# Performance work log

Measured on AMD Instinct MI355X. Metric: run time of the kernel, lower is better.

## Reference

```python
import jax, jax.numpy as jnp
import numpy as np

NUM_CODE = 256
DIM_CODE = 64
IMG_DIM = 3 * 32 * 32  # 3072
HID = 16384


def vq(x, codebook, noise_level, key):
    # x: [B, 64], codebook: [256, 64]
    # torch.cdist p=2 -> euclidean distances [B, 256]
    x2 = jnp.sum(x * x, axis=1, keepdims=True)            # [B,1]
    c2 = jnp.sum(codebook * codebook, axis=1)             # [256]
    d = jnp.sqrt(jnp.maximum(x2 - 2.0 * (x @ codebook.T) + c2, 0.0))
    r = jax.nn.softmax(-d / jnp.sqrt(jnp.float32(DIM_CODE)), axis=1)
    noise = jax.random.uniform(key, r.shape, dtype=r.dtype)
    idx = jnp.argmax(r - noise_level * noise, axis=1)
    one_hot = jax.nn.one_hot(idx, NUM_CODE, dtype=r.dtype)
    # straight-through: forward = one_hot, grad flows through r
    r_ste = r - jax.lax.stop_gradient(r - one_hot)
    return r_ste @ codebook                               # [B, 64]


def setup_inputs() -> dict:
    key = jax.random.key(0)
    ks = jax.random.split(key, 10)
    B = 4096
    inp = {
        "x": jax.random.normal(ks[0], (B, 3, 32, 32), dtype=jnp.float32),
        "wb1_encoder": jax.random.normal(ks[1], (IMG_DIM + 1, HID), dtype=jnp.float32) / np.sqrt(IMG_DIM).astype(np.float32),
        "wb2_encoder": jax.random.normal(ks[2], (HID + 1, 4 * DIM_CODE), dtype=jnp.float32) / 128.0,
        "wb1_decoder": jax.random.normal(ks[3], (4 * DIM_CODE + 1, HID), dtype=jnp.float32) / np.sqrt(4 * DIM_CODE).astype(np.float32),
        "wb2_decoder": jax.random.normal(ks[4], (HID + 1, IMG_DIM), dtype=jnp.float32) / 128.0,
        "codebook1": jax.random.normal(ks[5], (NUM_CODE, DIM_CODE), dtype=jnp.float32),
        "codebook2": jax.random.normal(ks[6], (NUM_CODE, DIM_CODE), dtype=jnp.float32),
        "codebook3": jax.random.normal(ks[7], (NUM_CODE, DIM_CODE), dtype=jnp.float32),
        "codebook4": jax.random.normal(ks[8], (NUM_CODE, DIM_CODE), dtype=jnp.float32),
        "noise_level": 1,
    }
    return inp


def reference(x, wb1_encoder, wb2_encoder, wb1_decoder, wb2_decoder,
              codebook1, codebook2, codebook3, codebook4, noise_level):
    nkey = jax.random.key(12345)
    h = jnp.tanh(x.reshape(-1, IMG_DIM) @ wb1_encoder[:-1] + wb1_encoder[-1])
    h = jnp.tanh(h @ wb2_encoder[:-1] + wb2_encoder[-1])      # [B, 256]
    x1, x2, x3, x4 = jnp.split(h, 4, axis=1)                  # each [B, 64]
    # NOTE: source uses codebook1 for all four chunks (faithful to original)
    y1 = vq(x1, codebook1, noise_level, jax.random.fold_in(nkey, 1))
    y2 = vq(x2, codebook1, noise_level, jax.random.fold_in(nkey, 2))
    y3 = vq(x3, codebook1, noise_level, jax.random.fold_in(nkey, 3))
    y4 = vq(x4, codebook1, noise_level, jax.random.fold_in(nkey, 4))
    y = jnp.concatenate((y1, y2, y3, y4), axis=1)             # [B, 256]
    y = jnp.tanh(y @ wb1_decoder[:-1] + wb1_decoder[-1])
    y = y @ wb2_decoder[:-1] + wb2_decoder[-1]
    return y.reshape(-1, 3, 32, 32)
```

## Files before the change

### kernel.cpp

```cpp
#include <hip/hip_runtime.h>
#include <stdint.h>


#define IMG_DIM 3072
#define HID     16384
#define NCODE   256
#define DCODE   64

typedef short bf16x8 __attribute__((ext_vector_type(8)));
typedef float f32x4 __attribute__((ext_vector_type(4)));

__device__ __forceinline__ uint16_t bf16rne(float f) {
    uint32_t u = __float_as_uint(f);
    return (uint16_t)((u + 0x7fffu + ((u >> 16) & 1u)) >> 16);
}
__device__ __forceinline__ float b2f(uint16_t h) {
    return __uint_as_float((uint32_t)h << 16);
}

#define GLLDS(g, l)                                                        \
    __builtin_amdgcn_global_load_lds(                                      \
        (const __attribute__((address_space(1))) uint32_t*)(const void*)(g), \
        (__attribute__((address_space(3))) uint32_t*)(void*)(l), 16, 0, 0)

__host__ __device__ __forceinline__ uint32_t rotl32(uint32_t v, int d) {
    return (v << d) | (v >> (32 - d));
}

__host__ __device__ __forceinline__ void tf2x32(uint32_t k0, uint32_t k1,
                                                uint32_t& x0, uint32_t& x1) {
    uint32_t k2 = k0 ^ k1 ^ 0x1BD11BDAu;
    x0 += k0; x1 += k1;
    x0 += x1; x1 = rotl32(x1, 13); x1 ^= x0;
    x0 += x1; x1 = rotl32(x1, 15); x1 ^= x0;
    x0 += x1; x1 = rotl32(x1, 26); x1 ^= x0;
    x0 += x1; x1 = rotl32(x1,  6); x1 ^= x0;
    x0 += k1; x1 += k2 + 1u;
    x0 += x1; x1 = rotl32(x1, 17); x1 ^= x0;
    x0 += x1; x1 = rotl32(x1, 29); x1 ^= x0;
    x0 += x1; x1 = rotl32(x1, 16); x1 ^= x0;
    x0 += x1; x1 = rotl32(x1, 24); x1 ^= x0;
    x0 += k2; x1 += k0 + 2u;
    x0 += x1; x1 = rotl32(x1, 13); x1 ^= x0;
    x0 += x1; x1 = rotl32(x1, 15); x1 ^= x0;
    x0 += x1; x1 = rotl32(x1, 26); x1 ^= x0;
    x0 += x1; x1 = rotl32(x1,  6); x1 ^= x0;
    x0 += k0; x1 += k1 + 3u;
    x0 += x1; x1 = rotl32(x1, 17); x1 ^= x0;
    x0 += x1; x1 = rotl32(x1, 29); x1 ^= x0;
    x0 += x1; x1 = rotl32(x1, 16); x1 ^= x0;
    x0 += x1; x1 = rotl32(x1, 24); x1 ^= x0;
    x0 += k1; x1 += k2 + 4u;
    x0 += x1; x1 = rotl32(x1, 13); x1 ^= x0;
    x0 += x1; x1 = rotl32(x1, 15); x1 ^= x0;
    x0 += x1; x1 = rotl32(x1, 26); x1 ^= x0;
    x0 += x1; x1 = rotl32(x1,  6); x1 ^= x0;
    x0 += k2; x1 += k0 + 5u;
}

template <int EPI, bool SPLIT>
__global__ __launch_bounds__(256) void gemm_mfma(
    const uint16_t* __restrict__ Ahi, const uint16_t* __restrict__ Alo,
    const uint16_t* __restrict__ Bhi, const uint16_t* __restrict__ Blo,
    const float* __restrict__ biasp,
    float* __restrict__ Cf, uint16_t* __restrict__ Cb,
    uint16_t* __restrict__ Chi, uint16_t* __restrict__ Clo,
    int M, int N, int K) {
    constexpr int AT = 128 * 32;
    __shared__ __align__(16) uint16_t As[SPLIT ? 2 * AT : AT];
    __shared__ __align__(16) uint16_t Bs[SPLIT ? 2 * AT : AT];

    const int tid = threadIdx.x;
    const int lane = tid & 63, wv = tid >> 6;
    const int wm = wv >> 1, wn = wv & 1;
    const int la = lane & 15, lk = lane >> 4;
    const size_t bm = (size_t)blockIdx.y * 128, bn = (size_t)blockIdx.x * 128;

    f32x4 acc[4][4];
#pragma unroll
    for (int i = 0; i < 4; ++i)
#pragma unroll
        for (int j = 0; j < 4; ++j) acc[i][j] = (f32x4){0.f, 0.f, 0.f, 0.f};

    for (int k0 = 0; k0 < K; k0 += 32) {
#pragma unroll
        for (int t = 0; t < 2; ++t) {
            const int cb_ = wv * 128 + t * 64;
            const int c = cb_ + lane;
            const int row = c >> 2, sub = c & 3;
            GLLDS(Ahi + (bm + row) * (size_t)K + k0 + sub * 8, &As[(size_t)cb_ * 8]);
            GLLDS(Bhi + (bn + row) * (size_t)K + k0 + sub * 8, &Bs[(size_t)cb_ * 8]);
            if constexpr (SPLIT) {
                GLLDS(Alo + (bm + row) * (size_t)K + k0 + sub * 8, &As[AT + (size_t)cb_ * 8]);
                GLLDS(Blo + (bn + row) * (size_t)K + k0 + sub * 8, &Bs[AT + (size_t)cb_ * 8]);
            }
        }
        __syncthreads();

        bf16x8 ah[4], bh[4], al[4], bl[4];
#pragma unroll
        for (int i = 0; i < 4; ++i) {
            const int ao = (wm * 64 + i * 16 + la) * 32 + lk * 8;
            const int bo = (wn * 64 + i * 16 + la) * 32 + lk * 8;
            ah[i] = *(const bf16x8*)&As[ao];
            bh[i] = *(const bf16x8*)&Bs[bo];
            if constexpr (SPLIT) {
                al[i] = *(const bf16x8*)&As[AT + ao];
                bl[i] = *(const bf16x8*)&Bs[AT + bo];
            }
        }
#pragma unroll
        for (int i = 0; i < 4; ++i)
#pragma unroll
            for (int j = 0; j < 4; ++j) {
                acc[i][j] = __builtin_amdgcn_mfma_f32_16x16x32_bf16(ah[i], bh[j], acc[i][j], 0, 0, 0);
                if constexpr (SPLIT) {
                    acc[i][j] = __builtin_amdgcn_mfma_f32_16x16x32_bf16(al[i], bh[j], acc[i][j], 0, 0, 0);
                    acc[i][j] = __builtin_amdgcn_mfma_f32_16x16x32_bf16(ah[i], bl[j], acc[i][j], 0, 0, 0);
                }
            }
        __syncthreads();
    }

    const int colb = (int)bn + wn * 64 + la;
    float bj[4];
#pragma unroll
    for (int j = 0; j < 4; ++j) bj[j] = biasp[colb + j * 16];
#pragma unroll
    for (int i = 0; i < 4; ++i) {
        const int rb = (int)bm + wm * 64 + i * 16 + lk * 4;
#pragma unroll
        for (int j = 0; j < 4; ++j) {
            const int col = colb + j * 16;
#pragma unroll
            for (int r = 0; r < 4; ++r) {
                float v = acc[i][j][r] + bj[j];
                const size_t idx = (size_t)(rb + r) * N + col;
                if constexpr (EPI == 0) Cf[idx] = v;
                if constexpr (EPI == 1) Cf[idx] = tanhf(v);
                if constexpr (EPI == 2) Cb[idx] = bf16rne(tanhf(v));
                if constexpr (EPI == 3) {
                    float tv = tanhf(v);
                    uint16_t h = bf16rne(tv);
                    Chi[idx] = h;
                    Clo[idx] = bf16rne(tv - b2f(h));
                }
            }
        }
    }
}

template <bool SPLIT>
__global__ __launch_bounds__(256) void wconv(const float* __restrict__ W,
                                             uint16_t* __restrict__ Thi,
                                             uint16_t* __restrict__ Tlo,
                                             int K, int N) {
    __shared__ float t[32][33];
    const int k0 = blockIdx.x * 32, n0 = blockIdx.y * 32;
    const int tid = threadIdx.x;
    {
        const int kl = tid >> 3, nq = tid & 7;
        float4 v = *(const float4*)(W + (size_t)(k0 + kl) * N + n0 + nq * 4);
        t[kl][nq * 4 + 0] = v.x;
        t[kl][nq * 4 + 1] = v.y;
        t[kl][nq * 4 + 2] = v.z;
        t[kl][nq * 4 + 3] = v.w;
    }
    __syncthreads();
    {
        const int nl = tid >> 3, kq = tid & 7;
        ushort4 hv, lv;
        float f0 = t[kq * 4 + 0][nl], f1 = t[kq * 4 + 1][nl];
        float f2 = t[kq * 4 + 2][nl], f3 = t[kq * 4 + 3][nl];
        hv.x = bf16rne(f0); hv.y = bf16rne(f1); hv.z = bf16rne(f2); hv.w = bf16rne(f3);
        *(ushort4*)(Thi + (size_t)(n0 + nl) * K + k0 + kq * 4) = hv;
        if constexpr (SPLIT) {
            lv.x = bf16rne(f0 - b2f(hv.x)); lv.y = bf16rne(f1 - b2f(hv.y));
            lv.z = bf16rne(f2 - b2f(hv.z)); lv.w = bf16rne(f3 - b2f(hv.w));
            *(ushort4*)(Tlo + (size_t)(n0 + nl) * K + k0 + kq * 4) = lv;
        }
    }
}

__global__ __launch_bounds__(256) void split_x(const float* __restrict__ x,
                                               uint16_t* __restrict__ hi,
                                               uint16_t* __restrict__ lo,
                                               size_t n4) {
    for (size_t i = (size_t)blockIdx.x * 256 + threadIdx.x; i < n4;
         i += (size_t)gridDim.x * 256) {
        float4 v = ((const float4*)x)[i];
        ushort4 h, l;
        h.x = bf16rne(v.x); l.x = bf16rne(v.x - b2f(h.x));
        h.y = bf16rne(v.y); l.y = bf16rne(v.y - b2f(h.y));
        h.z = bf16rne(v.z); l.z = bf16rne(v.z - b2f(h.z));
        h.w = bf16rne(v.w); l.w = bf16rne(v.w - b2f(h.w));
        ((ushort4*)hi)[i] = h;
        ((ushort4*)lo)[i] = l;
    }
}

template <bool YB16>
__global__ __launch_bounds__(256) void vq_kernel(
    const float* __restrict__ h, const float* __restrict__ cb,
    const uint32_t* __restrict__ nlp,
    float* __restrict__ yf, uint16_t* __restrict__ yb,
    uint32_t ka0, uint32_t ka1, uint32_t kb0, uint32_t kb1,
    uint32_t kc0, uint32_t kc1, uint32_t kd0, uint32_t kd1) {
    __shared__ float xs[DCODE];
    __shared__ float sred[NCODE];
    __shared__ int sidx[NCODE];

    const int b = blockIdx.x;
    const int chunk = blockIdx.y;
    const int c = threadIdx.x;

    if (c < DCODE) xs[c] = h[(size_t)b * NCODE + chunk * DCODE + c];
    __syncthreads();

    float dot = 0.f, x2 = 0.f, c2 = 0.f;
    const float* crow = cb + c * DCODE;
#pragma unroll 8
    for (int i = 0; i < DCODE; ++i) {
        float xv = xs[i], cv = crow[i];
        dot = fmaf(xv, cv, dot);
        x2 = fmaf(xv, xv, x2);
        c2 = fmaf(cv, cv, c2);
    }
    float d = sqrtf(fmaxf(x2 - 2.f * dot + c2, 0.f));
    float logit = -d * 0.125f;

    sred[c] = logit;
    __syncthreads();
    for (int s = 128; s > 0; s >>= 1) {
        if (c < s) sred[c] = fmaxf(sred[c], sred[c + s]);
        __syncthreads();
    }
    float mx = sred[0];
    __syncthreads();
    float e = expf(logit - mx);
    sred[c] = e;
    __syncthreads();
    for (int s = 128; s > 0; s >>= 1) {
        if (c < s) sred[c] = sred[c] + sred[c + s];
        __syncthreads();
    }
    float ssum = sred[0];
    __syncthreads();
    float r = e / ssum;

    int vi = (int)nlp[0];
    float noise_level = (vi >= -1000000 && vi <= 1000000)
                            ? (float)vi
                            : __uint_as_float(nlp[0]);

    uint32_t lin = (uint32_t)b * 256u + (uint32_t)c;
    uint32_t k0 = chunk == 0 ? ka0 : chunk == 1 ? kb0 : chunk == 2 ? kc0 : kd0;
    uint32_t k1 = chunk == 0 ? ka1 : chunk == 1 ? kb1 : chunk == 2 ? kc1 : kd1;
    uint32_t x0 = 0u, x1 = lin;
    tf2x32(k0, k1, x0, x1);
    uint32_t bits = x0 ^ x1;
    float noise = __uint_as_float((bits >> 9) | 0x3f800000u) - 1.0f;

    float score = r - noise_level * noise;

    sred[c] = score;
    sidx[c] = c;
    __syncthreads();
    for (int s = 128; s > 0; s >>= 1) {
        if (c < s) {
            float ov = sred[c + s];
            int oi = sidx[c + s];
            if (ov > sred[c] || (ov == sred[c] && oi < sidx[c])) {
                sred[c] = ov;
                sidx[c] = oi;
            }
        }
        __syncthreads();
    }
    int best = sidx[0];

    if (c < DCODE) {
        float v = cb[(size_t)best * DCODE + c];
        if constexpr (YB16)
            yb[(size_t)b * NCODE + chunk * DCODE + c] = bf16rne(v);
        else
            yf[(size_t)b * NCODE + chunk * DCODE + c] = v;
    }
}

template <int BM, int BN, bool TANH>
__global__ __launch_bounds__(256) void gemm_f32(const float* __restrict__ A,
                                                const float* __restrict__ W,
                                                float* __restrict__ C,
                                                int M, int N, int K) {
    constexpr int BK = 16;
    constexpr int TM = BM / 16, TN = BN / 16;
    constexpr int GM = TM / 4, GN = TN / 4;
    constexpr int PA = BM + 4, PB = BN + 4;
    __shared__ float As[BK][PA];
    __shared__ float Bs[BK][PB];

    const int tid = threadIdx.x;
    const int tx = tid & 15, ty = tid >> 4;
    const size_t bm = (size_t)blockIdx.y * BM;
    const size_t bn = (size_t)blockIdx.x * BN;

    float acc[TM][TN];
#pragma unroll
    for (int i = 0; i < TM; ++i)
#pragma unroll
        for (int j = 0; j < TN; ++j) acc[i][j] = 0.f;

    for (int k0 = 0; k0 < K; k0 += BK) {
#pragma unroll
        for (int i = 0; i < BM * BK / 4 / 256; ++i) {
            int f4 = tid + i * 256;
            int row = f4 >> 2;
            int c4 = f4 & 3;
            float4 v = *reinterpret_cast<const float4*>(A + (bm + row) * K + k0 + c4 * 4);
            As[c4 * 4 + 0][row] = v.x;
            As[c4 * 4 + 1][row] = v.y;
            As[c4 * 4 + 2][row] = v.z;
            As[c4 * 4 + 3][row] = v.w;
        }
#pragma unroll
        for (int i = 0; i < BK * BN / 4 / 256; ++i) {
            int f4 = tid + i * 256;
            int row = f4 / (BN / 4);
            int c4 = f4 % (BN / 4);
            *reinterpret_cast<float4*>(&Bs[row][c4 * 4]) =
                *reinterpret_cast<const float4*>(W + (size_t)(k0 + row) * N + bn + c4 * 4);
        }
        __syncthreads();
#pragma unroll
        for (int k = 0; k < BK; ++k) {
            float4 af[GM], bf[GN];
#pragma unroll
            for (int g = 0; g < GM; ++g)
                af[g] = *reinterpret_cast<const float4*>(&As[k][g * 64 + ty * 4]);
#pragma unroll
            for (int g = 0; g < GN; ++g)
                bf[g] = *reinterpret_cast<const float4*>(&Bs[k][g * 64 + tx * 4]);
#pragma unroll
            for (int gm = 0; gm < GM; ++gm) {
                const float* ap = &af[gm].x;
#pragma unroll
                for (int r = 0; r < 4; ++r) {
#pragma unroll
                    for (int gn = 0; gn < GN; ++gn) {
                        const float* bp = &bf[gn].x;
#pragma unroll
                        for (int c = 0; c < 4; ++c)
                            acc[gm * 4 + r][gn * 4 + c] =
                                fmaf(ap[r], bp[c], acc[gm * 4 + r][gn * 4 + c]);
                    }
                }
            }
        }
        __syncthreads();
    }

#pragma unroll
    for (int gm = 0; gm < GM; ++gm) {
#pragma unroll
        for (int r = 0; r < 4; ++r) {
            size_t row = bm + gm * 64 + ty * 4 + r;
#pragma unroll
            for (int gn = 0; gn < GN; ++gn) {
                size_t col = bn + gn * 64 + tx * 4;
                float4 bias = *reinterpret_cast<const float4*>(W + (size_t)K * N + col);
                float4 o;
                o.x = acc[gm * 4 + r][gn * 4 + 0] + bias.x;
                o.y = acc[gm * 4 + r][gn * 4 + 1] + bias.y;
                o.z = acc[gm * 4 + r][gn * 4 + 2] + bias.z;
                o.w = acc[gm * 4 + r][gn * 4 + 3] + bias.w;
                if (TANH) {
                    o.x = tanhf(o.x); o.y = tanhf(o.y);
                    o.z = tanhf(o.z); o.w = tanhf(o.w);
                }
                *reinterpret_cast<float4*>(C + row * N + col) = o;
            }
        }
    }
}

extern "C" void kernel_launch(void* const* d_in, const int* in_sizes, int n_in,
                              void* d_out, int out_size, void* d_ws, size_t ws_size,
                              hipStream_t stream) {
    const float* x   = (const float*)d_in[0];
    const float* w1e = (const float*)d_in[1];
    const float* w2e = (const float*)d_in[2];
    const float* w1d = (const float*)d_in[3];
    const float* w2d = (const float*)d_in[4];
    const float* cb1 = (const float*)d_in[5];
    const uint32_t* nl = (const uint32_t*)d_in[9];
    float* out = (float*)d_out;

    const int M = in_sizes[0] / IMG_DIM;

    uint32_t ks[4][2];
    for (int j = 1; j <= 4; ++j) {
        uint32_t a = 0u, bb = (uint32_t)j;
        tf2x32(0u, 12345u, a, bb);
        ks[j - 1][0] = a;
        ks[j - 1][1] = bb;
    }

    const size_t o_h1hi  = 0;
    const size_t o_h1lo  = 134217728;
    const size_t o_w1ehi = 268435456;
    const size_t o_w1elo = 369098752;
    const size_t o_w2ehi = 469762048;
    const size_t o_w2elo = 478150656;
    const size_t o_h     = 486539264;
    const size_t o_y     = 490733568;
    const size_t o_xhi   = 492830720;
    const size_t o_xlo   = 517996544;
    const size_t NEED    = 543162368;

    uint8_t* ws = (uint8_t*)d_ws;

    if (ws_size >= NEED) {
        uint16_t* h1hi  = (uint16_t*)(ws + o_h1hi);
        uint16_t* h1lo  = (uint16_t*)(ws + o_h1lo);
        uint16_t* w1ehi = (uint16_t*)(ws + o_w1ehi);
        uint16_t* w1elo = (uint16_t*)(ws + o_w1elo);
        uint16_t* w2ehi = (uint16_t*)(ws + o_w2ehi);
        uint16_t* w2elo = (uint16_t*)(ws + o_w2elo);
        float*    hbuf  = (float*)(ws + o_h);
        uint16_t* ybuf  = (uint16_t*)(ws + o_y);
        uint16_t* xhi   = (uint16_t*)(ws + o_xhi);
        uint16_t* xlo   = (uint16_t*)(ws + o_xlo);
        uint16_t* wt2d  = (uint16_t*)(ws + o_w1ehi);
        uint16_t* wt1d  = (uint16_t*)(ws + o_w1elo);
        uint16_t* h2    = (uint16_t*)(ws + o_h1hi);

        split_x<<<2048, 256, 0, stream>>>(x, xhi, xlo, (size_t)M * IMG_DIM / 4);
        wconv<true><<<dim3(IMG_DIM / 32, HID / 32), 256, 0, stream>>>(w1e, w1ehi, w1elo, IMG_DIM, HID);
        wconv<true><<<dim3(HID / 32, NCODE / 32), 256, 0, stream>>>(w2e, w2ehi, w2elo, HID, NCODE);
        gemm_mfma<3, true><<<dim3(HID / 128, M / 128), 256, 0, stream>>>(
            xhi, xlo, w1ehi, w1elo, w1e + (size_t)IMG_DIM * HID,
            nullptr, nullptr, h1hi, h1lo, M, HID, IMG_DIM);
        wconv<false><<<dim3(HID / 32, IMG_DIM / 32), 256, 0, stream>>>(w2d, wt2d, nullptr, HID, IMG_DIM);
        wconv<false><<<dim3(NCODE / 32, HID / 32), 256, 0, stream>>>(w1d, wt1d, nullptr, NCODE, HID);
        gemm_mfma<1, true><<<dim3(NCODE / 128, M / 128), 256, 0, stream>>>(
            h1hi, h1lo, w2ehi, w2elo, w2e + (size_t)HID * NCODE,
            hbuf, nullptr, nullptr, nullptr, M, NCODE, HID);
        vq_kernel<true><<<dim3(M, 4), 256, 0, stream>>>(
            hbuf, cb1, nl, nullptr, ybuf,
            ks[0][0], ks[0][1], ks[1][0], ks[1][1],
            ks[2][0], ks[2][1], ks[3][0], ks[3][1]);
        gemm_mfma<2, false><<<dim3(HID / 128, M / 128), 256, 0, stream>>>(
            ybuf, nullptr, wt1d, nullptr, w1d + (size_t)NCODE * HID,
            nullptr, h2, nullptr, nullptr, M, HID, NCODE);
        gemm_mfma<0, false><<<dim3(IMG_DIM / 128, M / 128), 256, 0, stream>>>(
            h2, nullptr, wt2d, nullptr, w2d + (size_t)HID * IMG_DIM,
            out, nullptr, nullptr, nullptr, M, IMG_DIM, HID);
    } else {
        float* h1 = (float*)d_ws;
        float* h  = h1 + (size_t)M * HID;
        float* yb = h + (size_t)M * NCODE;
        {
            dim3 g(HID / 128, M / 128);
            gemm_f32<128, 128, true><<<g, 256, 0, stream>>>(x, w1e, h1, M, HID, IMG_DIM);
        }
        {
            dim3 g(NCODE / 64, M / 64);
            gemm_f32<64, 64, true><<<g, 256, 0, stream>>>(h1, w2e, h, M, NCODE, HID);
        }
        vq_kernel<false><<<dim3(M, 4), 256, 0, stream>>>(
            h, cb1, nl, yb, nullptr,
            ks[0][0], ks[0][1], ks[1][0], ks[1][1],
            ks[2][0], ks[2][1], ks[3][0], ks[3][1]);
        {
            dim3 g(HID / 128, M / 128);
            gemm_f32<128, 128, true><<<g, 256, 0, stream>>>(yb, w1d, h1, M, HID, NCODE);
        }
        {
            dim3 g(IMG_DIM / 128, M / 128);
            gemm_f32<128, 128, false><<<g, 256, 0, stream>>>(h1, w2d, out, M, IMG_DIM, HID);
        }
    }
}
```

Baseline: 3.088 ms.

## Add 256x256 eight-wave pipelined bf16x3 GEMM for encoder layer one

```diff
diff --git a/kernel.cpp b/kernel.cpp
--- a/kernel.cpp
+++ b/kernel.cpp
@@ -58,6 +58,152 @@
     x0 += k2; x1 += k0 + 5u;
 }
 
+template <int EPI, int TPS, int NSEG>
+__global__ __launch_bounds__(512) void gemm8p(
+    const uint16_t* __restrict__ a0, const uint16_t* __restrict__ a1,
+    const uint16_t* __restrict__ a2,
+    const uint16_t* __restrict__ b0, const uint16_t* __restrict__ b1,
+    const uint16_t* __restrict__ b2,
+    const float* __restrict__ biasp,
+    float* __restrict__ Cf, uint16_t* __restrict__ Cb,
+    uint16_t* __restrict__ Chi, uint16_t* __restrict__ Clo,
+    int N, int Kseg) {
+    __shared__ __align__(16) uint8_t lds[131072];
+    constexpr int NT = TPS * NSEG;
+
+    const int tid = threadIdx.x;
+    const int lane = tid & 63, wv = tid >> 6;
+    const int wm = wv >> 2, wn = wv & 3;
+    const int la = lane & 15;
+    const int lkb = (lane >> 4) << 4;
+
+    const int nbx = gridDim.x;
+    const int nwg = nbx * gridDim.y;
+    int flat = blockIdx.y * nbx + blockIdx.x;
+    if ((nwg & 7) == 0) flat = (flat & 7) * (nwg >> 3) + (flat >> 3);
+    const size_t bm = (size_t)(flat / nbx) * 256;
+    const size_t bn = (size_t)(flat % nbx) * 256;
+
+    auto swz = [](int r) -> int {
+        return (((r >> 1) & 1) << 5) | (((r >> 2) & 1) << 4);
+    };
+
+    auto stage = [&](int tt, int mat, int kh) {
+        if (tt >= NT) return;
+        const int s = tt / TPS;
+        const int tloc = tt - s * TPS;
+        const uint16_t* mb;
+        size_t rb;
+        if (mat == 0) { mb = (s == 0 ? a0 : (s == 1 ? a1 : a2)); rb = bm; }
+        else          { mb = (s == 0 ? b0 : (s == 1 ? b1 : b2)); rb = bn; }
+        const int ub = mat * 65536 + (tt & 1) * 32768 + kh * 16384;
+#pragma unroll
+        for (int p = 0; p < 2; ++p) {
+            const int off = (p * 512 + tid) * 16;
+            const int r = off >> 6;
+            const int logc = (off & 63) ^ swz(r);
+            const uint16_t* src =
+                mb + (rb + r) * (size_t)Kseg + tloc * 64 + kh * 32 + (logc >> 1);
+            GLLDS(src, lds + ub + p * 8192 + wv * 1024);
+        }
+    };
+
+    auto rdA = [&](int buf, int ks, int i) -> bf16x8 {
+        const int r = wm * 128 + i * 16 + la;
+        return *(const bf16x8*)(lds + buf * 32768 + ks * 16384 + r * 64 +
+                                (lkb ^ swz(r)));
+    };
+    auto rdB = [&](int buf, int ks, int j) -> bf16x8 {
+        const int r = wn * 64 + j * 16 + la;
+        return *(const bf16x8*)(lds + 65536 + buf * 32768 + ks * 16384 + r * 64 +
+                                (lkb ^ swz(r)));
+    };
+
+    f32x4 acc[8][4];
+#pragma unroll
+    for (int i = 0; i < 8; ++i)
+#pragma unroll
+        for (int j = 0; j < 4; ++j) acc[i][j] = (f32x4){0.f, 0.f, 0.f, 0.f};
+
+    stage(0, 0, 0); stage(0, 1, 0); stage(0, 0, 1); stage(0, 1, 1);
+    stage(1, 0, 0); stage(1, 1, 0);
+    __builtin_amdgcn_sched_barrier(0);
+    if (NT > 1) asm volatile("s_waitcnt vmcnt(4)" ::: "memory");
+    else        asm volatile("s_waitcnt vmcnt(0)" ::: "memory");
+    __builtin_amdgcn_sched_barrier(0);
+    __builtin_amdgcn_s_barrier();
+    __builtin_amdgcn_sched_barrier(0);
+
+    for (int tt = 0; tt < NT; ++tt) {
+        const int buf = tt & 1;
+        bf16x8 b[4];
+#pragma unroll
+        for (int ph = 0; ph < 4; ++ph) {
+            const int ks = ph >> 1, ih = ph & 1;
+            bf16x8 a[4];
+#pragma unroll
+            for (int ii = 0; ii < 4; ++ii) a[ii] = rdA(buf, ks, ih * 4 + ii);
+            if (ih == 0) {
+#pragma unroll
+                for (int j = 0; j < 4; ++j) b[j] = rdB(buf, ks, j);
+            }
+            if (ph == 0) stage(tt + 1, 0, 1);
+            else if (ph == 1) stage(tt + 1, 1, 1);
+            else if (ph == 2) stage(tt + 2, 0, 0);
+            else stage(tt + 2, 1, 0);
+            __builtin_amdgcn_sched_barrier(0);
+            __builtin_amdgcn_s_barrier();
+            __builtin_amdgcn_sched_barrier(0);
+            __builtin_amdgcn_s_setprio(1);
+#pragma unroll
+            for (int ii = 0; ii < 4; ++ii)
+#pragma unroll
+                for (int j = 0; j < 4; ++j)
+                    acc[ih * 4 + ii][j] = __builtin_amdgcn_mfma_f32_16x16x32_bf16(
+                        a[ii], b[j], acc[ih * 4 + ii][j], 0, 0, 0);
+            __builtin_amdgcn_s_setprio(0);
+            __builtin_amdgcn_sched_barrier(0);
+            if (ph < 3) {
+                __builtin_amdgcn_s_barrier();
+                __builtin_amdgcn_sched_barrier(0);
+            } else {
+                if (tt + 2 < NT) asm volatile("s_waitcnt vmcnt(4)" ::: "memory");
+                else             asm volatile("s_waitcnt vmcnt(0)" ::: "memory");
+                __builtin_amdgcn_sched_barrier(0);
+                __builtin_amdgcn_s_barrier();
+                __builtin_amdgcn_sched_barrier(0);
+            }
+        }
+    }
+
+    const int colb = (int)bn + wn * 64 + la;
+    float bj[4];
+#pragma unroll
+    for (int j = 0; j < 4; ++j) bj[j] = biasp[colb + j * 16];
+#pragma unroll
+    for (int i = 0; i < 8; ++i) {
+        const int rb = (int)bm + wm * 128 + i * 16 + (lane >> 4) * 4;
+#pragma unroll
+        for (int j = 0; j < 4; ++j) {
+            const int col = colb + j * 16;
+#pragma unroll
+            for (int r = 0; r < 4; ++r) {
+                float v = acc[i][j][r] + bj[j];
+                const size_t idx = (size_t)(rb + r) * N + col;
+                if constexpr (EPI == 0) Cf[idx] = v;
+                if constexpr (EPI == 1) Cf[idx] = tanhf(v);
+                if constexpr (EPI == 2) Cb[idx] = bf16rne(tanhf(v));
+                if constexpr (EPI == 3) {
+                    float tv = tanhf(v);
+                    uint16_t h = bf16rne(tv);
+                    Chi[idx] = h;
+                    Clo[idx] = bf16rne(tv - b2f(h));
+                }
+            }
+        }
+    }
+}
+
 template <int EPI, bool SPLIT>
 __global__ __launch_bounds__(256) void gemm_mfma(
     const uint16_t* __restrict__ Ahi, const uint16_t* __restrict__ Alo,
@@ -438,9 +584,10 @@
         split_x<<<2048, 256, 0, stream>>>(x, xhi, xlo, (size_t)M * IMG_DIM / 4);
         wconv<true><<<dim3(IMG_DIM / 32, HID / 32), 256, 0, stream>>>(w1e, w1ehi, w1elo, IMG_DIM, HID);
         wconv<true><<<dim3(HID / 32, NCODE / 32), 256, 0, stream>>>(w2e, w2ehi, w2elo, HID, NCODE);
-        gemm_mfma<3, true><<<dim3(HID / 128, M / 128), 256, 0, stream>>>(
-            xhi, xlo, w1ehi, w1elo, w1e + (size_t)IMG_DIM * HID,
-            nullptr, nullptr, h1hi, h1lo, M, HID, IMG_DIM);
+        gemm8p<3, 48, 3><<<dim3(HID / 256, M / 256), 512, 0, stream>>>(
+            xhi, xlo, xhi, w1ehi, w1ehi, w1elo,
+            w1e + (size_t)IMG_DIM * HID,
+            nullptr, nullptr, h1hi, h1lo, HID, IMG_DIM);
         wconv<false><<<dim3(HID / 32, IMG_DIM / 32), 256, 0, stream>>>(w2d, wt2d, nullptr, HID, IMG_DIM);
         wconv<false><<<dim3(NCODE / 32, HID / 32), 256, 0, stream>>>(w1d, wt1d, nullptr, NCODE, HID);
         gemm_mfma<1, true><<<dim3(NCODE / 128, M / 128), 256, 0, stream>>>(
```

Result: slower. 4.182 ms (+35.4%).

## Split-K the encoder second GEMM and fuse partial reduction with tanh into VQ

Applied to the files above, without the earlier changes.

```diff
diff --git a/kernel.cpp b/kernel.cpp
--- a/kernel.cpp
+++ b/kernel.cpp
@@ -58,14 +58,14 @@
     x0 += k2; x1 += k0 + 5u;
 }
 
-template <int EPI, bool SPLIT>
+template <int EPI, bool SPLIT, bool KSPLIT>
 __global__ __launch_bounds__(256) void gemm_mfma(
     const uint16_t* __restrict__ Ahi, const uint16_t* __restrict__ Alo,
     const uint16_t* __restrict__ Bhi, const uint16_t* __restrict__ Blo,
     const float* __restrict__ biasp,
     float* __restrict__ Cf, uint16_t* __restrict__ Cb,
     uint16_t* __restrict__ Chi, uint16_t* __restrict__ Clo,
-    int M, int N, int K) {
+    int M, int N, int K, int lda, int ldb) {
     constexpr int AT = 128 * 32;
     __shared__ __align__(16) uint16_t As[SPLIT ? 2 * AT : AT];
     __shared__ __align__(16) uint16_t Bs[SPLIT ? 2 * AT : AT];
@@ -76,6 +76,16 @@
     const int la = lane & 15, lk = lane >> 4;
     const size_t bm = (size_t)blockIdx.y * 128, bn = (size_t)blockIdx.x * 128;
 
+    int kc = 0;
+    if constexpr (KSPLIT) {
+        kc = blockIdx.z;
+        const size_t ko = (size_t)kc * K;
+        Ahi += ko;
+        Bhi += ko;
+        if constexpr (SPLIT) { Alo += ko; Blo += ko; }
+        Cf += (size_t)kc * M * N;
+    }
+
     f32x4 acc[4][4];
 #pragma unroll
     for (int i = 0; i < 4; ++i)
@@ -88,11 +98,11 @@
             const int cb_ = wv * 128 + t * 64;
             const int c = cb_ + lane;
             const int row = c >> 2, sub = c & 3;
-            GLLDS(Ahi + (bm + row) * (size_t)K + k0 + sub * 8, &As[(size_t)cb_ * 8]);
-            GLLDS(Bhi + (bn + row) * (size_t)K + k0 + sub * 8, &Bs[(size_t)cb_ * 8]);
+            GLLDS(Ahi + (bm + row) * (size_t)lda + k0 + sub * 8, &As[(size_t)cb_ * 8]);
+            GLLDS(Bhi + (bn + row) * (size_t)ldb + k0 + sub * 8, &Bs[(size_t)cb_ * 8]);
             if constexpr (SPLIT) {
-                GLLDS(Alo + (bm + row) * (size_t)K + k0 + sub * 8, &As[AT + (size_t)cb_ * 8]);
-                GLLDS(Blo + (bn + row) * (size_t)K + k0 + sub * 8, &Bs[AT + (size_t)cb_ * 8]);
+                GLLDS(Alo + (bm + row) * (size_t)lda + k0 + sub * 8, &As[AT + (size_t)cb_ * 8]);
+                GLLDS(Blo + (bn + row) * (size_t)ldb + k0 + sub * 8, &Bs[AT + (size_t)cb_ * 8]);
             }
         }
         __syncthreads();
@@ -126,6 +136,12 @@
     float bj[4];
 #pragma unroll
     for (int j = 0; j < 4; ++j) bj[j] = biasp[colb + j * 16];
+    if constexpr (KSPLIT) {
+        if (kc != 0) {
+#pragma unroll
+            for (int j = 0; j < 4; ++j) bj[j] = 0.f;
+        }
+    }
 #pragma unroll
     for (int i = 0; i < 4; ++i) {
         const int rb = (int)bm + wm * 64 + i * 16 + lk * 4;
@@ -199,9 +215,10 @@
     }
 }
 
-template <bool YB16>
+template <bool YB16, int NPART>
 __global__ __launch_bounds__(256) void vq_kernel(
-    const float* __restrict__ h, const float* __restrict__ cb,
+    const float* __restrict__ h, size_t pstride,
+    const float* __restrict__ cb,
     const uint32_t* __restrict__ nlp,
     float* __restrict__ yf, uint16_t* __restrict__ yb,
     uint32_t ka0, uint32_t ka1, uint32_t kb0, uint32_t kb1,
@@ -214,7 +231,17 @@
     const int chunk = blockIdx.y;
     const int c = threadIdx.x;
 
-    if (c < DCODE) xs[c] = h[(size_t)b * NCODE + chunk * DCODE + c];
+    if (c < DCODE) {
+        const size_t idx = (size_t)b * NCODE + chunk * DCODE + c;
+        if constexpr (NPART > 0) {
+            float z = h[idx];
+#pragma unroll
+            for (int p = 1; p < NPART; ++p) z += h[(size_t)p * pstride + idx];
+            xs[c] = tanhf(z);
+        } else {
+            xs[c] = h[idx];
+        }
+    }
     __syncthreads();
 
     float dot = 0.f, x2 = 0.f, c2 = 0.f;
@@ -427,35 +454,35 @@
         uint16_t* w1elo = (uint16_t*)(ws + o_w1elo);
         uint16_t* w2ehi = (uint16_t*)(ws + o_w2ehi);
         uint16_t* w2elo = (uint16_t*)(ws + o_w2elo);
-        float*    hbuf  = (float*)(ws + o_h);
         uint16_t* ybuf  = (uint16_t*)(ws + o_y);
         uint16_t* xhi   = (uint16_t*)(ws + o_xhi);
         uint16_t* xlo   = (uint16_t*)(ws + o_xlo);
         uint16_t* wt2d  = (uint16_t*)(ws + o_w1ehi);
         uint16_t* wt1d  = (uint16_t*)(ws + o_w1elo);
         uint16_t* h2    = (uint16_t*)(ws + o_h1hi);
+        float*    e2p   = (float*)(ws + o_xhi);
 
         split_x<<<2048, 256, 0, stream>>>(x, xhi, xlo, (size_t)M * IMG_DIM / 4);
         wconv<true><<<dim3(IMG_DIM / 32, HID / 32), 256, 0, stream>>>(w1e, w1ehi, w1elo, IMG_DIM, HID);
         wconv<true><<<dim3(HID / 32, NCODE / 32), 256, 0, stream>>>(w2e, w2ehi, w2elo, HID, NCODE);
-        gemm_mfma<3, true><<<dim3(HID / 128, M / 128), 256, 0, stream>>>(
+        gemm_mfma<3, true, false><<<dim3(HID / 128, M / 128), 256, 0, stream>>>(
             xhi, xlo, w1ehi, w1elo, w1e + (size_t)IMG_DIM * HID,
-            nullptr, nullptr, h1hi, h1lo, M, HID, IMG_DIM);
+            nullptr, nullptr, h1hi, h1lo, M, HID, IMG_DIM, IMG_DIM, IMG_DIM);
         wconv<false><<<dim3(HID / 32, IMG_DIM / 32), 256, 0, stream>>>(w2d, wt2d, nullptr, HID, IMG_DIM);
         wconv<false><<<dim3(NCODE / 32, HID / 32), 256, 0, stream>>>(w1d, wt1d, nullptr, NCODE, HID);
-        gemm_mfma<1, true><<<dim3(NCODE / 128, M / 128), 256, 0, stream>>>(
+        gemm_mfma<0, true, true><<<dim3(NCODE / 128, M / 128, 4), 256, 0, stream>>>(
             h1hi, h1lo, w2ehi, w2elo, w2e + (size_t)HID * NCODE,
-            hbuf, nullptr, nullptr, nullptr, M, NCODE, HID);
-        vq_kernel<true><<<dim3(M, 4), 256, 0, stream>>>(
-            hbuf, cb1, nl, nullptr, ybuf,
+            e2p, nullptr, nullptr, nullptr, M, NCODE, HID / 4, HID, HID);
+        vq_kernel<true, 4><<<dim3(M, 4), 256, 0, stream>>>(
+            e2p, (size_t)M * NCODE, cb1, nl, nullptr, ybuf,
             ks[0][0], ks[0][1], ks[1][0], ks[1][1],
             ks[2][0], ks[2][1], ks[3][0], ks[3][1]);
-        gemm_mfma<2, false><<<dim3(HID / 128, M / 128), 256, 0, stream>>>(
+        gemm_mfma<2, false, false><<<dim3(HID / 128, M / 128), 256, 0, stream>>>(
             ybuf, nullptr, wt1d, nullptr, w1d + (size_t)NCODE * HID,
-            nullptr, h2, nullptr, nullptr, M, HID, NCODE);
-        gemm_mfma<0, false><<<dim3(IMG_DIM / 128, M / 128), 256, 0, stream>>>(
+            nullptr, h2, nullptr, nullptr, M, HID, NCODE, NCODE, NCODE);
+        gemm_mfma<0, false, false><<<dim3(IMG_DIM / 128, M / 128), 256, 0, stream>>>(
             h2, nullptr, wt2d, nullptr, w2d + (size_t)HID * IMG_DIM,
-            out, nullptr, nullptr, nullptr, M, IMG_DIM, HID);
+            out, nullptr, nullptr, nullptr, M, IMG_DIM, HID, HID, HID);
     } else {
         float* h1 = (float*)d_ws;
         float* h  = h1 + (size_t)M * HID;
@@ -468,8 +495,8 @@
             dim3 g(NCODE / 64, M / 64);
             gemm_f32<64, 64, true><<<g, 256, 0, stream>>>(h1, w2e, h, M, NCODE, HID);
         }
-        vq_kernel<false><<<dim3(M, 4), 256, 0, stream>>>(
-            h, cb1, nl, yb, nullptr,
+        vq_kernel<false, 0><<<dim3(M, 4), 256, 0, stream>>>(
+            h, 0, cb1, nl, yb, nullptr,
             ks[0][0], ks[0][1], ks[1][0], ks[1][1],
             ks[2][0], ks[2][1], ks[3][0], ks[3][1]);
         {
```

After: 2.551 ms. 17.4% less time.
